# Optimization experiments

Hardware: AMD Instinct MI355X
Metric: run time of the kernel (lower is better)

Reference implementation:

```python
import jax, jax.numpy as jnp
import numpy as np

N = 20000   # nodes
E = 160000  # edges
D = 128     # out_dim == in_dim
H = 8       # heads
DK = D // H # 16


def setup_inputs() -> dict:
    key = jax.random.key(0)
    ks = jax.random.split(key, 16)
    f = lambda i, shape, s=1.0: jax.random.normal(ks[i], shape, dtype=jnp.float32) * s
    z = lambda shape: jnp.zeros(shape, dtype=jnp.float32)
    return {
        "x_txt": f(0, (N, D)), "x_img": f(1, (N, D)), "x_s": f(2, (N, D)),
        "Wk": f(3, (D, D), 0.05), "bk": z((D,)),
        "Wq": f(4, (D, D), 0.05), "bq": z((D,)),
        "Wv": f(5, (D, D), 0.05), "bv": z((D,)),
        "Wa": f(6, (D, D), 0.05), "ba": z((D,)),
        "rel_att": f(7, (H, DK, DK), 0.25),
        "rel_msg": f(8, (H, DK, DK), 0.25),
        "rel_pri": jnp.ones((H,), jnp.float32),
        "wm_txt": f(9, (H, DK, DK), 0.25),
        "wm_img": f(10, (H, DK, DK), 0.25),
        "wm_s": f(11, (H, DK, DK), 0.25),
        "skip": jnp.ones((1,), jnp.float32),
        "src": jax.random.randint(ks[12], (E,), 0, N),
        "dst": jax.random.randint(ks[13], (E,), 0, N),
    }


def reference(x_txt, x_img, x_s, Wk, bk, Wq, bq, Wv, bv, Wa, ba,
              rel_att, rel_msg, rel_pri, wm_txt, wm_img, wm_s, skip, src, dst):
    n_heads, dk = rel_att.shape[0], rel_att.shape[1]
    n_nodes = x_txt.shape[0]
    sqrt_dk = jnp.sqrt(jnp.asarray(dk, jnp.float32))

    def proj(x, W, b):
        return (x @ W + b).reshape(n_nodes, n_heads, dk)

    xs = (x_txt, x_img, x_s)
    k = [proj(x, Wk, bk)[src] for x in xs]  # [E,H,dk] gathered at src
    q = [proj(x, Wq, bq)[dst] for x in xs]  # [E,H,dk] gathered at dst
    v = [proj(x, Wv, bv)[src] for x in xs]

    # cross-modal lambda: per-edge modality alignment softmax (over the 3 modalities)
    wm = (wm_txt, wm_img, wm_s)
    lam_scores = jnp.stack(
        [jnp.einsum('ehd,hdf,ehf->eh', k[m], wm[m], q[m]) for m in range(3)], axis=0)
    lam = jax.nn.softmax(lam_scores, axis=0)  # [3,E,H]

    # edge attention logits (scaled *10 as in reduce_func) and relation-msg values
    att = [jnp.einsum('ehd,hdf,ehf->eh', k[m], rel_att, q[m]) * rel_pri / sqrt_dk * 10.0
           for m in range(3)]
    vmsg = [jnp.einsum('ehd,hdf->ehf', v[m], rel_msg) for m in range(3)]

    align = -(jnp.abs(att[0] - att[1]) + jnp.abs(att[0] - att[2])
              + jnp.abs(att[1] - att[2])) / 3.0

    def seg_softmax(x):  # softmax over edges sharing the same dst node
        m = jax.ops.segment_max(x, dst, num_segments=n_nodes)
        m = jnp.where(jnp.isfinite(m), m, 0.0)
        e = jnp.exp(x - m[dst])
        s = jax.ops.segment_sum(e, dst, num_segments=n_nodes)
        s = jnp.where(s == 0.0, 1.0, s)
        return e / s[dst]

    beta2 = seg_softmax(align)
    sm = [seg_softmax(a) for a in att]
    beta1 = sm[0] * lam[0] + sm[1] * lam[1] + sm[2] * lam[2]
    beta = seg_softmax(beta1 * beta2)  # [E,H]

    alpha = jax.nn.sigmoid(skip)  # [1]
    outs = []
    for m in range(3):
        h = jax.ops.segment_sum(beta[..., None] * vmsg[m], dst,
                                num_segments=n_nodes).reshape(n_nodes, -1)
        outs.append((h @ Wa + ba) * alpha + xs[m] * (1.0 - alpha))
    return tuple(outs)
```

## Files before the change

### kernel.cpp

```cpp
#include <hip/hip_runtime.h>

#define D 128
#define NH 8

typedef __bf16 bf16x8 __attribute__((ext_vector_type(8)));
typedef unsigned short ushortx8 __attribute__((ext_vector_type(8)));
typedef float floatx4 __attribute__((ext_vector_type(4)));

__device__ __forceinline__ float bf2f(unsigned short u) {
  union { unsigned int i; float f; } x; x.i = ((unsigned int)u) << 16; return x.f;
}
__device__ __forceinline__ unsigned short f2bf(float f) {
  union { float f; unsigned int i; } x; x.f = f;
  unsigned int i = x.i;
  return (unsigned short)((i + 0x7FFFu + ((i >> 16) & 1u)) >> 16);
}
__device__ __forceinline__ void acc2(unsigned int ku, unsigned int qu, float& s) {
  union { unsigned int i; float f; } a, b;
  a.i = ku << 16;          b.i = qu << 16;          s += a.f * b.f;
  a.i = ku & 0xffff0000u;  b.i = qu & 0xffff0000u;  s += a.f * b.f;
}

__global__ void k_zero(float* __restrict__ p, long long n) {
  long long i = ((long long)blockIdx.x * blockDim.x + threadIdx.x) * 4;
  long long stride = (long long)gridDim.x * blockDim.x * 4;
  for (; i + 3 < n; i += stride) {
    *(float4*)(p + i) = make_float4(0.f, 0.f, 0.f, 0.f);
  }
}

__global__ __launch_bounds__(256) void k_transform(
    const float* __restrict__ Wk, const float* __restrict__ bk,
    const float* __restrict__ Wq, const float* __restrict__ bq,
    const float* __restrict__ Wv, const float* __restrict__ bv,
    const float* __restrict__ rel_att, const float* __restrict__ rel_msg,
    const float* __restrict__ rel_pri,
    const float* __restrict__ wm0, const float* __restrict__ wm1,
    const float* __restrict__ wm2,
    unsigned short* __restrict__ Wt_all, float* __restrict__ bias_all)
{
  int gid = blockIdx.x * 256 + threadIdx.x;
  if (gid >= 6 * 128 * 128) return;
  int p = gid >> 14;
  int idx = gid & 16383;
  int c = idx >> 7, k = idx & 127;
  int h = c >> 4, r = c & 15;
  float wsum = 0.f, bsum = 0.f;
  if (p == 0) {
    wsum = Wk[k * 128 + c];
    bsum = bk[c];
  } else if (p <= 4) {
    const float* M = (p == 1) ? rel_att : ((p == 2) ? wm0 : ((p == 3) ? wm1 : wm2));
#pragma unroll
    for (int f = 0; f < 16; f++) {
      float mv = M[h * 256 + r * 16 + f];
      wsum += Wq[k * 128 + h * 16 + f] * mv;
      bsum += bq[h * 16 + f] * mv;
    }
    if (p == 1) { float sc = rel_pri[h] * 2.5f; wsum *= sc; bsum *= sc; }
  } else {
#pragma unroll
    for (int d = 0; d < 16; d++) {
      float mv = rel_msg[h * 256 + d * 16 + r];
      wsum += Wv[k * 128 + h * 16 + d] * mv;
      bsum += bv[h * 16 + d] * mv;
    }
  }
  Wt_all[(size_t)p * 16384 + c * 128 + k] = f2bf(wsum);
  if (k == 0) bias_all[p * 128 + c] = bsum;
}

__global__ __launch_bounds__(256) void k_proj(
    const float* __restrict__ x0, const float* __restrict__ x1,
    const float* __restrict__ x2,
    const unsigned short* __restrict__ Wt_all, const float* __restrict__ bias_all,
    unsigned short* __restrict__ P, int N)
{
  __shared__ __attribute__((aligned(16))) unsigned short Wt[128 * 136];
  int m = blockIdx.y;
  const float* X = (m == 0) ? x0 : ((m == 1) ? x1 : x2);
  int tid = threadIdx.x;
  int wave = tid >> 6, lane = tid & 63;
  int quad = lane >> 4, l16 = lane & 15;
  int row0 = blockIdx.x * 64 + wave * 16;
  int arow = row0 + l16; if (arow >= N) arow = N - 1;
  const float* ap = X + (size_t)arow * D;
  bf16x8 afr[4];
#pragma unroll
  for (int kk4 = 0; kk4 < 4; kk4++) {
    float4 f0 = *(const float4*)(ap + kk4 * 32 + quad * 8);
    float4 f1 = *(const float4*)(ap + kk4 * 32 + quad * 8 + 4);
    ushortx8 uu;
    uu[0]=f2bf(f0.x); uu[1]=f2bf(f0.y); uu[2]=f2bf(f0.z); uu[3]=f2bf(f0.w);
    uu[4]=f2bf(f1.x); uu[5]=f2bf(f1.y); uu[6]=f2bf(f1.z); uu[7]=f2bf(f1.w);
    afr[kk4] = __builtin_bit_cast(bf16x8, uu);
  }
  for (int pt = 0; pt < 4; pt++) {
    int wp = (pt == 0) ? 0 : ((pt == 1) ? 1 : ((pt == 2) ? (2 + m) : 5));
    const unsigned short* Wsrc = Wt_all + (size_t)wp * 16384;
    const float* B = bias_all + wp * 128;
    __syncthreads();
    for (int idx = tid; idx < 128 * 128; idx += 256) {
      int c = idx >> 7, k = idx & 127;
      Wt[c * 136 + k] = Wsrc[idx];
    }
    __syncthreads();
    floatx4 acc[8];
#pragma unroll
    for (int ct = 0; ct < 8; ct++) acc[ct] = (floatx4)0.f;
#pragma unroll
    for (int kk4 = 0; kk4 < 4; kk4++) {
#pragma unroll
      for (int ct = 0; ct < 8; ct++) {
        uint4 bu = *(const uint4*)(&Wt[(ct * 16 + l16) * 136 + kk4 * 32 + quad * 8]);
        bf16x8 bf = __builtin_bit_cast(bf16x8, bu);
        acc[ct] = __builtin_amdgcn_mfma_f32_16x16x32_bf16(afr[kk4], bf, acc[ct], 0, 0, 0);
      }
    }
    unsigned short* Pout = P + (size_t)(pt * 3 + m) * N * D;
#pragma unroll
    for (int ct = 0; ct < 8; ct++) {
      int col = ct * 16 + l16;
      float bias = B[col];
#pragma unroll
      for (int i = 0; i < 4; i++) {
        int r = row0 + quad * 4 + i;
        if (r < N) Pout[(size_t)r * D + col] = f2bf(acc[ct][i] + bias);
      }
    }
  }
}

__global__ void k_hist(const int* __restrict__ dst, int* __restrict__ counts, int E) {
  int e = blockIdx.x * 256 + threadIdx.x;
  if (e < E) atomicAdd(&counts[dst[e]], 1);
}

__global__ __launch_bounds__(1024) void k_scan_part(
    const int* __restrict__ counts, int* __restrict__ row_start,
    int* __restrict__ partials, int N)
{
  __shared__ int wsum[16];
  int tid = threadIdx.x;
  int gi = blockIdx.x * 1024 + tid;
  int v = (gi < N) ? counts[gi] : 0;
  int lane = tid & 63, wid = tid >> 6;
  int x = v;
#pragma unroll
  for (int off = 1; off < 64; off <<= 1) {
    int y = __shfl_up(x, off, 64);
    if (lane >= off) x += y;
  }
  if (lane == 63) wsum[wid] = x;
  __syncthreads();
  if (wid == 0) {
    int ws = (lane < 16) ? wsum[lane] : 0;
#pragma unroll
    for (int off = 1; off < 16; off <<= 1) {
      int y = __shfl_up(ws, off, 64);
      if (lane >= off) ws += y;
    }
    if (lane < 16) wsum[lane] = ws;
  }
  __syncthreads();
  int excl = x - v + (wid > 0 ? wsum[wid - 1] : 0);
  if (gi <= N) row_start[gi] = excl;
  if (tid == 0) partials[blockIdx.x] = wsum[15];
}

__global__ __launch_bounds__(1024) void k_scan_fix(
    int* __restrict__ row_start, const int* __restrict__ partials, int N, int nb)
{
  __shared__ int offs[64];
  int tid = threadIdx.x;
  if (tid == 0) {
    int acc = 0;
    for (int b = 0; b < nb; b++) { offs[b] = acc; acc += partials[b]; }
  }
  __syncthreads();
  for (int i = tid; i <= N; i += 1024) row_start[i] += offs[i >> 10];
}

__global__ void k_scatter(const int* __restrict__ dst, const int* __restrict__ src,
                          const int* __restrict__ row_start,
                          int* __restrict__ cursor, int* __restrict__ src_sorted, int E) {
  int e = blockIdx.x * 256 + threadIdx.x;
  if (e < E) {
    int d = dst[e];
    int pos = atomicAdd(&cursor[d], 1);
    src_sorted[row_start[d] + pos] = src[e];
  }
}

__device__ __forceinline__ void edge_vals(
    const unsigned short* __restrict__ P, size_t Nsz, int s, int h,
    const uint4 (&qa)[3][2], const uint4 (&qw)[3][2],
    float (&av)[3], float (&lv)[3])
{
#pragma unroll
  for (int m = 0; m < 3; m++) {
    const unsigned short* kp = P + ((size_t)m * Nsz + s) * 128 + h * 16;
    uint4 k0 = *(const uint4*)kp, k1 = *(const uint4*)(kp + 8);
    const unsigned int* ka = (const unsigned int*)&k0;
    const unsigned int* kb = (const unsigned int*)&k1;
    const unsigned int* a0 = (const unsigned int*)&qa[m][0];
    const unsigned int* a1 = (const unsigned int*)&qa[m][1];
    const unsigned int* w0 = (const unsigned int*)&qw[m][0];
    const unsigned int* w1 = (const unsigned int*)&qw[m][1];
    float da = 0.f, dw = 0.f;
#pragma unroll
    for (int j = 0; j < 4; j++) {
      acc2(ka[j], a0[j], da); acc2(kb[j], a1[j], da);
      acc2(ka[j], w0[j], dw); acc2(kb[j], w1[j], dw);
    }
    av[m] = da;
    lv[m] = dw;
  }
  float mx = fmaxf(lv[0], fmaxf(lv[1], lv[2]));
  float e0 = __expf(lv[0] - mx), e1 = __expf(lv[1] - mx), e2 = __expf(lv[2] - mx);
  float inv = 1.f / (e0 + e1 + e2);
  lv[0] = e0 * inv; lv[1] = e1 * inv; lv[2] = e2 * inv;
}

__global__ __launch_bounds__(256) void k_node(
    const unsigned short* __restrict__ P,
    const int* __restrict__ row_start, const int* __restrict__ srcs,
    unsigned short* __restrict__ hagg, int N, int E)
{
  int tid = threadIdx.x;
  int wave = tid >> 6, lane = tid & 63;
  int n = blockIdx.x * 4 + wave;
  if (n >= N) return;
  int ro = row_start[n];
  int deg = row_start[n + 1] - ro;
  float acc00 = 0, acc01 = 0, acc10 = 0, acc11 = 0, acc20 = 0, acc21 = 0;
  if (deg > 0) {
    int h = lane & 7, slot = lane >> 3;
    size_t Nsz = (size_t)N;
    uint4 qa[3][2], qw[3][2];
#pragma unroll
    for (int m = 0; m < 3; m++) {
      const unsigned short* qap = P + ((size_t)(3 + m) * Nsz + n) * 128 + h * 16;
      const unsigned short* qwp = P + ((size_t)(6 + m) * Nsz + n) * 128 + h * 16;
      qa[m][0] = *(const uint4*)qap; qa[m][1] = *(const uint4*)(qap + 8);
      qw[m][0] = *(const uint4*)qwp; qw[m][1] = *(const uint4*)(qwp + 8);
    }
    int nch = (deg + 7) >> 3;
    float cX0[8] = {}, cX1[8] = {}, cX2[8] = {}, cEa[8] = {}, cT[8] = {};
    int cS[8] = {};
    float sA0 = 0, sA1 = 0, sA2 = 0, sAl = 0;
#pragma unroll
    for (int c = 0; c < 8; c++) {
      int idx = c * 8 + slot;
      if (c < nch && idx < deg) {
        int s = srcs[ro + idx]; cS[c] = s;
        float av[3], lv[3];
        edge_vals(P, Nsz, s, h, qa, qw, av, lv);
        float e0 = __expf(av[0]), e1 = __expf(av[1]), e2 = __expf(av[2]);
        float align = -(fabsf(av[0]-av[1]) + fabsf(av[0]-av[2]) + fabsf(av[1]-av[2])) * (1.f/3.f);
        float ea = __expf(align);
        cX0[c] = lv[0] * e0; cX1[c] = lv[1] * e1; cX2[c] = lv[2] * e2; cEa[c] = ea;
        sA0 += e0; sA1 += e1; sA2 += e2; sAl += ea;
      }
    }
    for (int c = 8; c < nch; c++) {
      int idx = c * 8 + slot;
      if (idx < deg) {
        int s = srcs[ro + idx];
        float av[3], lv[3];
        edge_vals(P, Nsz, s, h, qa, qw, av, lv);
        float align = -(fabsf(av[0]-av[1]) + fabsf(av[0]-av[2]) + fabsf(av[1]-av[2])) * (1.f/3.f);
        sA0 += __expf(av[0]); sA1 += __expf(av[1]); sA2 += __expf(av[2]);
        sAl += __expf(align);
      }
    }
#pragma unroll
    for (int off = 8; off < 64; off <<= 1) {
      sA0 += __shfl_xor(sA0, off, 64);
      sA1 += __shfl_xor(sA1, off, 64);
      sA2 += __shfl_xor(sA2, off, 64);
      sAl += __shfl_xor(sAl, off, 64);
    }
    float rA0 = 1.f / fmaxf(sA0, 1e-30f), rA1 = 1.f / fmaxf(sA1, 1e-30f);
    float rA2 = 1.f / fmaxf(sA2, 1e-30f), rAl = 1.f / fmaxf(sAl, 1e-30f);
    float sT = 0;
#pragma unroll
    for (int c = 0; c < 8; c++) {
      int idx = c * 8 + slot;
      if (c < nch && idx < deg) {
        float t = (cX0[c] * rA0 + cX1[c] * rA1 + cX2[c] * rA2) * (cEa[c] * rAl);
        cT[c] = t;
        sT += __expf(t);
      }
    }
    for (int c = 8; c < nch; c++) {
      int idx = c * 8 + slot;
      if (idx < deg) {
        int s = srcs[ro + idx];
        float av[3], lv[3];
        edge_vals(P, Nsz, s, h, qa, qw, av, lv);
        float align = -(fabsf(av[0]-av[1]) + fabsf(av[0]-av[2]) + fabsf(av[1]-av[2])) * (1.f/3.f);
        float t = (lv[0]*__expf(av[0])*rA0 + lv[1]*__expf(av[1])*rA1 + lv[2]*__expf(av[2])*rA2)
                  * (__expf(align) * rAl);
        sT += __expf(t);
      }
    }
#pragma unroll
    for (int off = 8; off < 64; off <<= 1) sT += __shfl_xor(sT, off, 64);
    float rT = 1.f / fmaxf(sT, 1e-30f);
    const unsigned int* Pu = (const unsigned int*)P;
    int hl = lane >> 3;
#pragma unroll
    for (int c = 0; c < 8; c++) {
      if (c < nch) {
        int idx = c * 8 + slot;
        float beta = (idx < deg) ? __expf(cT[c]) * rT : 0.f;
        int sv = cS[c];
        float bj[8]; int sj[8];
#pragma unroll
        for (int jj = 0; jj < 8; jj++) {
          bj[jj] = __shfl(beta, jj * 8 + hl, 64);
          sj[jj] = __shfl(sv, jj * 8, 64);
        }
#pragma unroll
        for (int jj = 0; jj < 8; jj++) {
          size_t base9 = ((size_t)9 * Nsz + sj[jj]) * 64 + lane;
          unsigned int u0 = Pu[base9];
          unsigned int u1 = Pu[base9 + Nsz * 64];
          unsigned int u2 = Pu[base9 + 2 * Nsz * 64];
          float b = bj[jj];
          acc00 += b * bf2f((unsigned short)u0); acc01 += b * bf2f((unsigned short)(u0 >> 16));
          acc10 += b * bf2f((unsigned short)u1); acc11 += b * bf2f((unsigned short)(u1 >> 16));
          acc20 += b * bf2f((unsigned short)u2); acc21 += b * bf2f((unsigned short)(u2 >> 16));
        }
      }
    }
    for (int c = 8; c < nch; c++) {
      int idx = c * 8 + slot;
      float beta = 0.f; int sv = 0;
      if (idx < deg) {
        sv = srcs[ro + idx];
        float av[3], lv[3];
        edge_vals(P, Nsz, sv, h, qa, qw, av, lv);
        float align = -(fabsf(av[0]-av[1]) + fabsf(av[0]-av[2]) + fabsf(av[1]-av[2])) * (1.f/3.f);
        float t = (lv[0]*__expf(av[0])*rA0 + lv[1]*__expf(av[1])*rA1 + lv[2]*__expf(av[2])*rA2)
                  * (__expf(align) * rAl);
        beta = __expf(t) * rT;
      }
      int jmax = min(8, deg - c * 8);
      for (int jj = 0; jj < jmax; jj++) {
        float b = __shfl(beta, jj * 8 + hl, 64);
        int s = __shfl(sv, jj * 8, 64);
        size_t base9 = ((size_t)9 * Nsz + s) * 64 + lane;
        unsigned int u0 = Pu[base9];
        unsigned int u1 = Pu[base9 + Nsz * 64];
        unsigned int u2 = Pu[base9 + 2 * Nsz * 64];
        acc00 += b * bf2f((unsigned short)u0); acc01 += b * bf2f((unsigned short)(u0 >> 16));
        acc10 += b * bf2f((unsigned short)u1); acc11 += b * bf2f((unsigned short)(u1 >> 16));
        acc20 += b * bf2f((unsigned short)u2); acc21 += b * bf2f((unsigned short)(u2 >> 16));
      }
    }
  }
  unsigned int* ho = (unsigned int*)hagg;
  ho[((size_t)0 * N + n) * 64 + lane] = ((unsigned int)f2bf(acc01) << 16) | f2bf(acc00);
  ho[((size_t)1 * N + n) * 64 + lane] = ((unsigned int)f2bf(acc11) << 16) | f2bf(acc10);
  ho[((size_t)2 * N + n) * 64 + lane] = ((unsigned int)f2bf(acc21) << 16) | f2bf(acc20);
}

__global__ __launch_bounds__(256) void k_out(
    const unsigned short* __restrict__ Hagg, const float* __restrict__ Wa,
    const float* __restrict__ ba,
    const float* __restrict__ x0, const float* __restrict__ x1,
    const float* __restrict__ x2, const float* __restrict__ skip,
    float* __restrict__ out, int N)
{
  __shared__ __attribute__((aligned(16))) unsigned short Wt[128 * 136];
  int m = blockIdx.y;
  const float* X = (m == 0) ? x0 : ((m == 1) ? x1 : x2);
  int tid = threadIdx.x;
  for (int idx = tid; idx < 128 * 128; idx += 256) {
    int k = idx >> 7, c = idx & 127;
    Wt[c * 136 + k] = f2bf(Wa[idx]);
  }
  __syncthreads();
  float alpha = 1.f / (1.f + __expf(-skip[0]));
  float oma = 1.f - alpha;
  int wave = tid >> 6, lane = tid & 63;
  int quad = lane >> 4, l16 = lane & 15;
  int row0 = blockIdx.x * 64 + wave * 16;
  int arow = row0 + l16; if (arow >= N) arow = N - 1;
  const unsigned short* hp = Hagg + ((size_t)m * N + arow) * D;
  floatx4 acc[8];
#pragma unroll
  for (int ct = 0; ct < 8; ct++) acc[ct] = (floatx4)0.f;
#pragma unroll
  for (int kk = 0; kk < 128; kk += 32) {
    uint4 au = *(const uint4*)(hp + kk + quad * 8);
    bf16x8 af = __builtin_bit_cast(bf16x8, au);
#pragma unroll
    for (int ct = 0; ct < 8; ct++) {
      uint4 bu = *(const uint4*)(&Wt[(ct * 16 + l16) * 136 + kk + quad * 8]);
      bf16x8 bf = __builtin_bit_cast(bf16x8, bu);
      acc[ct] = __builtin_amdgcn_mfma_f32_16x16x32_bf16(af, bf, acc[ct], 0, 0, 0);
    }
  }
  float* om = out + (size_t)m * N * D;
#pragma unroll
  for (int ct = 0; ct < 8; ct++) {
    int col = ct * 16 + l16;
    float bias = ba[col];
#pragma unroll
    for (int i = 0; i < 4; i++) {
      int r = row0 + quad * 4 + i;
      if (r < N) {
        om[(size_t)r * D + col] =
            (acc[ct][i] + bias) * alpha + X[(size_t)r * D + col] * oma;
      }
    }
  }
}

extern "C" void kernel_launch(void* const* d_in, const int* in_sizes, int n_in,
                              void* d_out, int out_size, void* d_ws, size_t ws_size,
                              hipStream_t stream) {
  const float* x0 = (const float*)d_in[0];
  const float* x1 = (const float*)d_in[1];
  const float* x2 = (const float*)d_in[2];
  const float* Wk = (const float*)d_in[3];
  const float* bk = (const float*)d_in[4];
  const float* Wq = (const float*)d_in[5];
  const float* bq = (const float*)d_in[6];
  const float* Wv = (const float*)d_in[7];
  const float* bv = (const float*)d_in[8];
  const float* Wa = (const float*)d_in[9];
  const float* ba = (const float*)d_in[10];
  const float* rel_att = (const float*)d_in[11];
  const float* rel_msg = (const float*)d_in[12];
  const float* rel_pri = (const float*)d_in[13];
  const float* wm0 = (const float*)d_in[14];
  const float* wm1 = (const float*)d_in[15];
  const float* wm2 = (const float*)d_in[16];
  const float* skip = (const float*)d_in[17];
  const int* src = (const int*)d_in[18];
  const int* dstv = (const int*)d_in[19];
  int N = in_sizes[0] / D;
  int E = in_sizes[18];

  char* wsb = (char*)d_ws;
  size_t off = 0;
  auto alloc = [&](size_t bytes) { size_t o = off; off += (bytes + 63) & ~(size_t)63; return o; };
  unsigned short* P         = (unsigned short*)(wsb + alloc((size_t)12 * N * D * 2));
  unsigned short* Wt_all    = (unsigned short*)(wsb + alloc((size_t)6 * 16384 * 2));
  float*          bias_all  = (float*)(wsb + alloc((size_t)6 * 128 * 4));
  int*            cnt2      = (int*)(wsb + alloc((size_t)2 * N * 4));
  int*            row_start = (int*)(wsb + alloc((size_t)(N + 1) * 4));
  int*            src_sorted= (int*)(wsb + alloc((size_t)E * 4));
  int*            partials  = (int*)(wsb + alloc((size_t)64 * 4));
  unsigned short* hagg      = (unsigned short*)(wsb + alloc((size_t)3 * N * D * 2));
  int* counts = cnt2;
  int* cursor = cnt2 + N;

  k_zero<<<dim3(40), 256, 0, stream>>>((float*)cnt2, (long long)2 * N);
  k_transform<<<dim3(384), 256, 0, stream>>>(
      Wk, bk, Wq, bq, Wv, bv, rel_att, rel_msg, rel_pri, wm0, wm1, wm2, Wt_all, bias_all);
  k_proj<<<dim3((N + 63) / 64, 3), 256, 0, stream>>>(
      x0, x1, x2, Wt_all, bias_all, P, N);
  k_hist<<<dim3((E + 255) / 256), 256, 0, stream>>>(dstv, counts, E);
  int nb = (N + 1024) / 1024;
  k_scan_part<<<dim3(nb), 1024, 0, stream>>>(counts, row_start, partials, N);
  k_scan_fix<<<dim3(1), 1024, 0, stream>>>(row_start, partials, N, nb);
  k_scatter<<<dim3((E + 255) / 256), 256, 0, stream>>>(dstv, src, row_start, cursor, src_sorted, E);
  k_node<<<dim3((N + 3) / 4), 256, 0, stream>>>(
      P, row_start, src_sorted, hagg, N, E);
  k_out<<<dim3((N + 63) / 64, 3), 256, 0, stream>>>(
      hagg, Wa, ba, x0, x1, x2, skip, (float*)d_out, N);
}
```

Before: 280.9 us.

## Merge histogram into weight-transform kernel, vectorize smem weight loads, shrink edge cache

```diff
diff --git a/kernel.cpp b/kernel.cpp
--- a/kernel.cpp
+++ b/kernel.cpp
@@ -21,15 +21,7 @@
   a.i = ku & 0xffff0000u;  b.i = qu & 0xffff0000u;  s += a.f * b.f;
 }
 
-__global__ void k_zero(float* __restrict__ p, long long n) {
-  long long i = ((long long)blockIdx.x * blockDim.x + threadIdx.x) * 4;
-  long long stride = (long long)gridDim.x * blockDim.x * 4;
-  for (; i + 3 < n; i += stride) {
-    *(float4*)(p + i) = make_float4(0.f, 0.f, 0.f, 0.f);
-  }
-}
-
-__global__ __launch_bounds__(256) void k_transform(
+__global__ __launch_bounds__(256) void k_misc(
     const float* __restrict__ Wk, const float* __restrict__ bk,
     const float* __restrict__ Wq, const float* __restrict__ bq,
     const float* __restrict__ Wv, const float* __restrict__ bv,
@@ -37,9 +29,16 @@
     const float* __restrict__ rel_pri,
     const float* __restrict__ wm0, const float* __restrict__ wm1,
     const float* __restrict__ wm2,
-    unsigned short* __restrict__ Wt_all, float* __restrict__ bias_all)
-{
-  int gid = blockIdx.x * 256 + threadIdx.x;
+    unsigned short* __restrict__ Wt_all, float* __restrict__ bias_all,
+    const int* __restrict__ dst, int* __restrict__ counts, int E)
+{
+  int b = blockIdx.x;
+  if (b >= 384) {
+    int e = (b - 384) * 256 + threadIdx.x;
+    if (e < E) atomicAdd(&counts[dst[e]], 1);
+    return;
+  }
+  int gid = b * 256 + threadIdx.x;
   if (gid >= 6 * 128 * 128) return;
   int p = gid >> 14;
   int idx = gid & 16383;
@@ -100,9 +99,11 @@
     const unsigned short* Wsrc = Wt_all + (size_t)wp * 16384;
     const float* B = bias_all + wp * 128;
     __syncthreads();
-    for (int idx = tid; idx < 128 * 128; idx += 256) {
-      int c = idx >> 7, k = idx & 127;
-      Wt[c * 136 + k] = Wsrc[idx];
+#pragma unroll
+    for (int it = 0; it < 8; it++) {
+      int idx = it * 256 + tid;
+      int c = idx >> 4, kc = (idx & 15) << 3;
+      *(uint4*)(&Wt[c * 136 + kc]) = *(const uint4*)(&Wsrc[c * 128 + kc]);
     }
     __syncthreads();
     floatx4 acc[8];
@@ -129,11 +130,6 @@
       }
     }
   }
-}
-
-__global__ void k_hist(const int* __restrict__ dst, int* __restrict__ counts, int E) {
-  int e = blockIdx.x * 256 + threadIdx.x;
-  if (e < E) atomicAdd(&counts[dst[e]], 1);
 }
 
 __global__ __launch_bounds__(1024) void k_scan_part(
@@ -246,11 +242,11 @@
       qw[m][0] = *(const uint4*)qwp; qw[m][1] = *(const uint4*)(qwp + 8);
     }
     int nch = (deg + 7) >> 3;
-    float cX0[8] = {}, cX1[8] = {}, cX2[8] = {}, cEa[8] = {}, cT[8] = {};
-    int cS[8] = {};
+    float cX0[4] = {}, cX1[4] = {}, cX2[4] = {}, cEa[4] = {}, cT[4] = {};
+    int cS[4] = {};
     float sA0 = 0, sA1 = 0, sA2 = 0, sAl = 0;
 #pragma unroll
-    for (int c = 0; c < 8; c++) {
+    for (int c = 0; c < 4; c++) {
       int idx = c * 8 + slot;
       if (c < nch && idx < deg) {
         int s = srcs[ro + idx]; cS[c] = s;
@@ -263,7 +259,7 @@
         sA0 += e0; sA1 += e1; sA2 += e2; sAl += ea;
       }
     }
-    for (int c = 8; c < nch; c++) {
+    for (int c = 4; c < nch; c++) {
       int idx = c * 8 + slot;
       if (idx < deg) {
         int s = srcs[ro + idx];
@@ -285,7 +281,7 @@
     float rA2 = 1.f / fmaxf(sA2, 1e-30f), rAl = 1.f / fmaxf(sAl, 1e-30f);
     float sT = 0;
 #pragma unroll
-    for (int c = 0; c < 8; c++) {
+    for (int c = 0; c < 4; c++) {
       int idx = c * 8 + slot;
       if (c < nch && idx < deg) {
         float t = (cX0[c] * rA0 + cX1[c] * rA1 + cX2[c] * rA2) * (cEa[c] * rAl);
@@ -293,7 +289,7 @@
         sT += __expf(t);
       }
     }
-    for (int c = 8; c < nch; c++) {
+    for (int c = 4; c < nch; c++) {
       int idx = c * 8 + slot;
       if (idx < deg) {
         int s = srcs[ro + idx];
@@ -311,7 +307,7 @@
     const unsigned int* Pu = (const unsigned int*)P;
     int hl = lane >> 3;
 #pragma unroll
-    for (int c = 0; c < 8; c++) {
+    for (int c = 0; c < 4; c++) {
       if (c < nch) {
         int idx = c * 8 + slot;
         float beta = (idx < deg) ? __expf(cT[c]) * rT : 0.f;
@@ -335,7 +331,7 @@
         }
       }
     }
-    for (int c = 8; c < nch; c++) {
+    for (int c = 4; c < nch; c++) {
       int idx = c * 8 + slot;
       float beta = 0.f; int sv = 0;
       if (idx < deg) {
@@ -378,9 +374,15 @@
   int m = blockIdx.y;
   const float* X = (m == 0) ? x0 : ((m == 1) ? x1 : x2);
   int tid = threadIdx.x;
-  for (int idx = tid; idx < 128 * 128; idx += 256) {
-    int k = idx >> 7, c = idx & 127;
-    Wt[c * 136 + k] = f2bf(Wa[idx]);
+#pragma unroll
+  for (int it = 0; it < 16; it++) {
+    int idx = it * 256 + tid;
+    int k = idx >> 5, c4 = (idx & 31) << 2;
+    float4 w = *(const float4*)(&Wa[k * 128 + c4]);
+    Wt[(c4 + 0) * 136 + k] = f2bf(w.x);
+    Wt[(c4 + 1) * 136 + k] = f2bf(w.y);
+    Wt[(c4 + 2) * 136 + k] = f2bf(w.z);
+    Wt[(c4 + 3) * 136 + k] = f2bf(w.w);
   }
   __syncthreads();
   float alpha = 1.f / (1.f + __expf(-skip[0]));
@@ -460,12 +462,13 @@
   int* counts = cnt2;
   int* cursor = cnt2 + N;
 
-  k_zero<<<dim3(40), 256, 0, stream>>>((float*)cnt2, (long long)2 * N);
-  k_transform<<<dim3(384), 256, 0, stream>>>(
-      Wk, bk, Wq, bq, Wv, bv, rel_att, rel_msg, rel_pri, wm0, wm1, wm2, Wt_all, bias_all);
+  hipMemsetAsync(cnt2, 0, (size_t)2 * N * sizeof(int), stream);
+  int hist_blocks = (E + 255) / 256;
+  k_misc<<<dim3(384 + hist_blocks), 256, 0, stream>>>(
+      Wk, bk, Wq, bq, Wv, bv, rel_att, rel_msg, rel_pri, wm0, wm1, wm2,
+      Wt_all, bias_all, dstv, counts, E);
   k_proj<<<dim3((N + 63) / 64, 3), 256, 0, stream>>>(
       x0, x1, x2, Wt_all, bias_all, P, N);
-  k_hist<<<dim3((E + 255) / 256), 256, 0, stream>>>(dstv, counts, E);
   int nb = (N + 1024) / 1024;
   k_scan_part<<<dim3(nb), 1024, 0, stream>>>(counts, row_start, partials, N);
   k_scan_fix<<<dim3(1), 1024, 0, stream>>>(row_start, partials, N, nb);
```

Result: faster. 256.3 us (-8.8%).
